# Optimization experiments

Hardware: AMD Instinct MI355X
Metric: run time of the kernel (lower is better)

Reference implementation:

```python
import jax, jax.numpy as jnp
import numpy as np

D_MODEL = 1024
N_HEADS = 16
D_K = D_MODEL // N_HEADS
THETA = 10000.0
B, S = 4, 2048


def setup_inputs() -> dict:
    key = jax.random.key(0)
    ks = jax.random.split(key, 5)
    scale = 0.02
    return {
        "x": jax.random.normal(ks[0], (B, S, D_MODEL), dtype=jnp.float32),
        "token_positions": jnp.arange(S, dtype=jnp.int32),
        "WQ": jax.random.normal(ks[1], (D_MODEL, D_MODEL), dtype=jnp.float32) * scale,
        "WK": jax.random.normal(ks[2], (D_MODEL, D_MODEL), dtype=jnp.float32) * scale,
        "WV": jax.random.normal(ks[3], (D_MODEL, D_MODEL), dtype=jnp.float32) * scale,
        "WO": jax.random.normal(ks[4], (D_MODEL, D_MODEL), dtype=jnp.float32) * scale,
    }


def apply_rope(x, positions):
    # x: [B, H, S, d_k]; rotate interleaved (even, odd) pairs
    half = D_K // 2
    inv_freq = THETA ** (-jnp.arange(half, dtype=x.dtype) * 2.0 / D_K)  # [half]
    ang = positions.astype(x.dtype)[:, None] * inv_freq[None, :]        # [S, half]
    cos, sin = jnp.cos(ang), jnp.sin(ang)
    x1 = x[..., 0::2]
    x2 = x[..., 1::2]
    r1 = x1 * cos - x2 * sin
    r2 = x1 * sin + x2 * cos
    return jnp.stack([r1, r2], axis=-1).reshape(x.shape)


def reference(x, token_positions, WQ, WK, WV, WO):
    b, s, _ = x.shape
    # Linear (no bias), weight stored (out, in): y = x @ W^T
    def proj(W):
        y = jnp.einsum('bsd,ed->bse', x, W)
        return y.reshape(b, s, N_HEADS, D_K).transpose(0, 2, 1, 3)  # [b,h,s,dk]
    Q, K, V = proj(WQ), proj(WK), proj(WV)
    Q = apply_rope(Q, token_positions)
    K = apply_rope(K, token_positions)
    scores = jnp.einsum('bhqd,bhkd->bhqk', Q, K) / jnp.sqrt(jnp.asarray(D_K, x.dtype))
    causal = jnp.tril(jnp.ones((s, s), dtype=bool))
    scores = jnp.where(causal, scores, -jnp.inf)
    attn = jax.nn.softmax(scores, axis=-1)
    out = jnp.einsum('bhqk,bhkd->bhqd', attn, V)
    out = out.transpose(0, 2, 1, 3).reshape(b, s, D_MODEL)
    return jnp.einsum('bse,de->bsd', out, WO)
```

## Files before the change

kernel.cpp:

```cpp
#include <hip/hip_runtime.h>
#include <cstdint>
#include <cstddef>

#define DM 1024
#define NH 16
#define DKD 64
#define BB 4
#define SS 2048
#define MTOT (BB*SS)

typedef float  f32x4  __attribute__((ext_vector_type(4)));
typedef __bf16 bf16x8 __attribute__((ext_vector_type(8)));
typedef __bf16 bf16x4v __attribute__((ext_vector_type(4)));
typedef __bf16 bf16x2v __attribute__((ext_vector_type(2)));
using as3v = __attribute__((address_space(3))) void;
using as1v = __attribute__((address_space(1))) void;

__device__ __forceinline__ void gl2lds16(const void* g, void* l) {
  __builtin_amdgcn_global_load_lds((as1v*)g, (as3v*)l, 16, 0, 0);
}

__device__ __forceinline__ float fast_exp2(float x) {
#if __has_builtin(__builtin_amdgcn_exp2f)
  return __builtin_amdgcn_exp2f(x);
#else
  return __expf(x * 0.6931471805599453f);
#endif
}

__device__ __forceinline__ void sincos_rev(float rev, float* s, float* c) {
#if __has_builtin(__builtin_amdgcn_sinf) && __has_builtin(__builtin_amdgcn_cosf)
  *s = __builtin_amdgcn_sinf(rev);
  *c = __builtin_amdgcn_cosf(rev);
#else
  float a = rev * 6.283185307179586f;
  *s = __sinf(a); *c = __cosf(a);
#endif
}

__device__ __forceinline__ uint32_t pkbf(float a, float b) {
  union { uint32_t u; __bf16 h[2]; } c;
  c.h[0] = (__bf16)a; c.h[1] = (__bf16)b;
  return c.u;
}

__global__ void cast_all_k(const float* __restrict__ x,
                           const float* __restrict__ wq, const float* __restrict__ wk,
                           const float* __restrict__ wv, const float* __restrict__ wo,
                           __bf16* __restrict__ xb,
                           __bf16* __restrict__ wqb, __bf16* __restrict__ wkb,
                           __bf16* __restrict__ wvb, __bf16* __restrict__ wob) {
  int i = blockIdx.x * blockDim.x + threadIdx.x;
  const float* src;
  __bf16* dst;
  int idx, oidx;
  if (i < 2097152) {
    src = x; dst = xb; idx = i; oidx = i;
  } else {
    int j = i - 2097152;
    int w = j >> 18;
    idx = j & 262143;
    src = (w == 0) ? wq : (w == 1) ? wk : (w == 2) ? wv : wo;
    dst = (w == 0) ? wqb : (w == 1) ? wkb : (w == 2) ? wvb : wob;
    if (w < 2) {
      int e = idx >> 8;
      int c = idx & 255;
      int d = e & 63;
      int dp = (d & 1) ? 32 + (d >> 1) : (d >> 1);
      oidx = (((e & ~63) | dp) << 8) | c;
    } else {
      oidx = idx;
    }
  }
  float4 f = ((const float4*)src)[idx];
  bf16x4v o;
  o[0] = (__bf16)f.x; o[1] = (__bf16)f.y; o[2] = (__bf16)f.z; o[3] = (__bf16)f.w;
  ((bf16x4v*)dst)[oidx] = o;
}

__global__ void rope_tbl_k(const int* __restrict__ pos, float2* __restrict__ tbl) {
  int p = blockIdx.x * blockDim.x + threadIdx.x;
  int s = p >> 5;
  int i = p & 31;
  float ps = (float)pos[s];
  float invr = __expf(-0.28782313663f * (float)i) * 0.15915494309f;
  float rev = ps * invr;
  rev -= floorf(rev);
  float sn, cs;
  sincos_rev(rev, &sn, &cs);
  tbl[p] = make_float2(cs, sn);
}

template <typename CT>
__global__ __launch_bounds__(256) void gemm_bt_k(const __bf16* __restrict__ A,
                                                 const __bf16* __restrict__ B,
                                                 CT* __restrict__ C,
                                                 int M, int N, int K) {
  __shared__ __bf16 As[128 * 32];
  __shared__ __bf16 Bs[128 * 32];
  const int tid  = threadIdx.x;
  const int lane = tid & 63;
  const int wid  = tid >> 6;
  const int lrow = lane & 15;
  const int quad = lane >> 4;
  const int m0 = blockIdx.y * 128;
  const int n0 = blockIdx.x * 128;
  const int wm = (wid & 1) * 64;
  const int wn = (wid >> 1) * 64;
  const int srow = wid * 32 + (lane >> 2);
  const int scol = (lane & 3) * 8;

  f32x4 acc[4][4] = {};

  for (int k0 = 0; k0 < K; k0 += 32) {
    __syncthreads();
    gl2lds16(A + (size_t)(m0 + srow)      * K + k0 + scol, As + (wid * 32)      * 32);
    gl2lds16(A + (size_t)(m0 + srow + 16) * K + k0 + scol, As + (wid * 32 + 16) * 32);
    gl2lds16(B + (size_t)(n0 + srow)      * K + k0 + scol, Bs + (wid * 32)      * 32);
    gl2lds16(B + (size_t)(n0 + srow + 16) * K + k0 + scol, Bs + (wid * 32 + 16) * 32);
    __syncthreads();

    bf16x8 af[4], bfr[4];
#pragma unroll
    for (int i = 0; i < 4; ++i)
      af[i] = *(const bf16x8*)(As + (wm + i * 16 + lrow) * 32 + quad * 8);
#pragma unroll
    for (int i = 0; i < 4; ++i)
      bfr[i] = *(const bf16x8*)(Bs + (wn + i * 16 + lrow) * 32 + quad * 8);
#pragma unroll
    for (int mi = 0; mi < 4; ++mi)
#pragma unroll
      for (int ni = 0; ni < 4; ++ni)
        acc[mi][ni] = __builtin_amdgcn_mfma_f32_16x16x32_bf16(af[mi], bfr[ni], acc[mi][ni], 0, 0, 0);
  }

#pragma unroll
  for (int mi = 0; mi < 4; ++mi)
#pragma unroll
    for (int ni = 0; ni < 4; ++ni)
#pragma unroll
      for (int r = 0; r < 4; ++r) {
        int row = m0 + wm + mi * 16 + quad * 4 + r;
        int col = n0 + wn + ni * 16 + lrow;
        C[(size_t)row * N + col] = (CT)acc[mi][ni][r];
      }
}

__global__ __launch_bounds__(256) void gemm_qkv_k(const __bf16* __restrict__ A,
                                                  const __bf16* __restrict__ Bq,
                                                  const __bf16* __restrict__ Bk,
                                                  const __bf16* __restrict__ Bv,
                                                  const float2* __restrict__ tbl,
                                                  __bf16* __restrict__ Cq,
                                                  __bf16* __restrict__ Ck,
                                                  __bf16* __restrict__ Cv) {
  __shared__ __bf16 As[128 * 32];
  __shared__ __bf16 Bs[128 * 32];
  const int sel = blockIdx.x >> 3;
  const __bf16* B = sel == 0 ? Bq : sel == 1 ? Bk : Bv;
  const int n0 = (blockIdx.x & 7) * 128;
  const int m0 = blockIdx.y * 128;
  const int K = DM;
  const int tid  = threadIdx.x;
  const int lane = tid & 63;
  const int wid  = tid >> 6;
  const int lrow = lane & 15;
  const int quad = lane >> 4;
  const int wm = (wid & 1) * 64;
  const int wn = (wid >> 1) * 64;
  const int srow = wid * 32 + (lane >> 2);
  const int scol = (lane & 3) * 8;

  f32x4 acc[4][4] = {};

  for (int k0 = 0; k0 < K; k0 += 32) {
    __syncthreads();
    gl2lds16(A + (size_t)(m0 + srow)      * K + k0 + scol, As + (wid * 32)      * 32);
    gl2lds16(A + (size_t)(m0 + srow + 16) * K + k0 + scol, As + (wid * 32 + 16) * 32);
    gl2lds16(B + (size_t)(n0 + srow)      * K + k0 + scol, Bs + (wid * 32)      * 32);
    gl2lds16(B + (size_t)(n0 + srow + 16) * K + k0 + scol, Bs + (wid * 32 + 16) * 32);
    __syncthreads();

    bf16x8 af[4], bfr[4];
#pragma unroll
    for (int i = 0; i < 4; ++i)
      af[i] = *(const bf16x8*)(As + (wm + i * 16 + lrow) * 32 + quad * 8);
#pragma unroll
    for (int i = 0; i < 4; ++i)
      bfr[i] = *(const bf16x8*)(Bs + (wn + i * 16 + lrow) * 32 + quad * 8);
#pragma unroll
    for (int mi = 0; mi < 4; ++mi)
#pragma unroll
      for (int ni = 0; ni < 4; ++ni)
        acc[mi][ni] = __builtin_amdgcn_mfma_f32_16x16x32_bf16(af[mi], bfr[ni], acc[mi][ni], 0, 0, 0);
  }

  const int hbase = (n0 + wn) >> 6;
  const int bq = m0 >> 11;

  if (sel == 2) {
    __bf16* vt = Cv + ((size_t)(bq * NH + hbase)) * (DKD * SS);
    const int S0 = (m0 + wm) & (SS - 1);
#pragma unroll
    for (int ni = 0; ni < 4; ++ni) {
      const int d = ni * 16 + lrow;
#pragma unroll
      for (int mi = 0; mi < 4; ++mi) {
        bf16x4v pk;
#pragma unroll
        for (int r = 0; r < 4; ++r) pk[r] = (__bf16)acc[mi][ni][r];
        const int sp = S0 + (mi >> 1) * 32 + quad * 8 + (mi & 1) * 4;
        *(bf16x4v*)(vt + (size_t)d * SS + sp) = pk;
      }
    }
  } else {
    __bf16* C = ((sel == 0) ? Cq : Ck) + ((size_t)(bq * NH + hbase)) * (SS * DKD);
#pragma unroll
    for (int ni = 0; ni < 2; ++ni) {
      const int i = ni * 16 + lrow;
#pragma unroll
      for (int mi = 0; mi < 4; ++mi) {
#pragma unroll
        for (int r = 0; r < 4; ++r) {
          int s = (m0 + wm + mi * 16 + quad * 4 + r) & (SS - 1);
          float2 cssn = tbl[s * 32 + i];
          float a = acc[mi][ni][r];
          float b = acc[mi][ni + 2][r];
          C[(size_t)s * DKD + i]      = (__bf16)fmaf(a, cssn.x, -(b * cssn.y));
          C[(size_t)s * DKD + 32 + i] = (__bf16)fmaf(a, cssn.y,  (b * cssn.x));
        }
      }
    }
  }
}

__global__ __launch_bounds__(512, 4) void attn9_k(const __bf16* __restrict__ Qh,
                                                  const __bf16* __restrict__ Kh,
                                                  const __bf16* __restrict__ VT,
                                                  __bf16* __restrict__ O) {
  __shared__ __bf16 Ks[2][128 * 64];
  __shared__ __bf16 Vt[2][64 * 128];
  const int tid  = threadIdx.x;
  const int lane = tid & 63;
  const int wid  = tid >> 6;
  const int lrow = lane & 15;
  const int quad = lane >> 4;
  const int j   = blockIdx.x;
  const int xcd = j & 7;
  const int t   = j >> 3;
  const int bh  = (xcd << 3) | (t >> 4);
  const int u   = t & 15;
  const int qi  = (u & 1) ? (u >> 1) : (15 - (u >> 1));
  const int b  = bh >> 4;
  const int h  = bh & 15;
  const int q0 = qi * 128;
  const size_t hb = (size_t)bh * (SS * DKD);
  const int qg = q0 + wid * 16 + lrow;

  bf16x8 qf0, qf1;
  {
    const __bf16* qp = Qh + hb + (size_t)qg * DKD + quad * 8;
    qf0 = *(const bf16x8*)qp;
    qf1 = *(const bf16x8*)(qp + 32);
  }
  f32x4 Oa[4] = {};
  float l = 0.f;
  const int nkt = qi + 1;

  const int skr = lane >> 3;
  const int skc = lane & 7;
  const int svd = lane >> 4;
  const int svc = lane & 15;

  auto stage = [&](int kt, int bsel) {
#pragma unroll
    for (int ii = 0; ii < 2; ++ii) {
      int i = wid * 2 + ii;
      int key = i * 8 + skr;
      int gc = skc ^ (key & 7);
      gl2lds16(Kh + hb + (size_t)(kt * 128 + key) * DKD + gc * 8, &Ks[bsel][i * 512]);
      int dk = i * 4 + svd;
      int gc2 = (svc & 8) | ((svc ^ dk) & 7);
      gl2lds16(VT + hb + (size_t)dk * SS + kt * 128 + gc2 * 8, &Vt[bsel][i * 512]);
    }
  };

  stage(0, 0);

  for (int kt = 0; kt < nkt; ++kt) {
    __syncthreads();
    if (kt + 1 < nkt) stage(kt + 1, (kt + 1) & 1);
    const __bf16* ks = Ks[kt & 1];
    const __bf16* vt = Vt[kt & 1];

    f32x4 sa[8];
#pragma unroll
    for (int mi = 0; mi < 8; ++mi) sa[mi] = (f32x4){0.f, 0.f, 0.f, 0.f};
    __builtin_amdgcn_s_setprio(1);
#pragma unroll
    for (int tt = 0; tt < 2; ++tt) {
      bf16x8 qf = tt ? qf1 : qf0;
#pragma unroll
      for (int mi = 0; mi < 8; ++mi) {
        bf16x8 kf = *(const bf16x8*)(ks + (mi * 16 + lrow) * 64 + (((tt * 4 + quad) ^ (lrow & 7)) * 8));
        sa[mi] = __builtin_amdgcn_mfma_f32_16x16x32_bf16(kf, qf, sa[mi], 0, 0, 0);
      }
    }
    __builtin_amdgcn_s_setprio(0);

    const bool lastt = (kt == nkt - 1);
#pragma unroll
    for (int kc = 0; kc < 4; ++kc) {
      union { uint32_t u[4]; bf16x8 v; } P;
#pragma unroll
      for (int half = 0; half < 2; ++half) {
        const int mi = kc * 2 + half;
        float pr[4];
#pragma unroll
        for (int r = 0; r < 4; ++r) {
          float p = fast_exp2(sa[mi][r] * 0.18033688f - 8.0f);
          if (lastt) {
            int key = kt * 128 + kc * 32 + half * 16 + quad * 4 + r;
            p = (key <= qg) ? p : 0.f;
          }
          l += p;
          pr[r] = p;
        }
        P.u[half * 2]     = pkbf(pr[0], pr[1]);
        P.u[half * 2 + 1] = pkbf(pr[2], pr[3]);
      }
      __builtin_amdgcn_s_setprio(1);
#pragma unroll
      for (int ni = 0; ni < 4; ++ni) {
        int c = kc * 4 + quad;
        int cp = (c & 8) | ((c ^ (lrow & 7)) & 7);
        bf16x8 vf = *(const bf16x8*)(vt + (ni * 16 + lrow) * 128 + cp * 8);
        Oa[ni] = __builtin_amdgcn_mfma_f32_16x16x32_bf16(P.v, vf, Oa[ni], 0, 0, 0);
      }
      __builtin_amdgcn_s_setprio(0);
    }
  }

  l += __shfl_xor(l, 16, 64);
  l += __shfl_xor(l, 32, 64);

#pragma unroll
  for (int r = 0; r < 4; ++r) {
    float li = __shfl(l, quad * 4 + r, 64);
    float inv = 1.0f / li;
    int row = q0 + wid * 16 + quad * 4 + r;
#pragma unroll
    for (int ni = 0; ni < 4; ++ni)
      O[(size_t)b * SS * DM + (size_t)row * DM + h * DKD + ni * 16 + lrow] =
          (__bf16)(Oa[ni][r] * inv);
  }
}

extern "C" void kernel_launch(void* const* d_in, const int* in_sizes, int n_in,
                              void* d_out, int out_size, void* d_ws, size_t ws_size,
                              hipStream_t stream) {
  (void)in_sizes; (void)n_in; (void)out_size; (void)ws_size;
  const float* x  = (const float*)d_in[0];
  const int*   pos = (const int*)d_in[1];
  const float* WQ = (const float*)d_in[2];
  const float* WK = (const float*)d_in[3];
  const float* WV = (const float*)d_in[4];
  const float* WO = (const float*)d_in[5];
  float* out = (float*)d_out;

  char* w = (char*)d_ws;
  const size_t MB = 1024 * 1024;
  __bf16* xb  = (__bf16*)(w);
  __bf16* wqb = (__bf16*)(w + 16 * MB);
  __bf16* wkb = (__bf16*)(w + 18 * MB);
  __bf16* wvb = (__bf16*)(w + 20 * MB);
  __bf16* wob = (__bf16*)(w + 22 * MB);
  __bf16* Qh  = (__bf16*)(w + 24 * MB);
  __bf16* Kh  = (__bf16*)(w + 40 * MB);
  __bf16* Cb  = (__bf16*)(w + 56 * MB);
  __bf16* VT  = (__bf16*)(w + 72 * MB);
  float2* tbl = (float2*)(w + 88 * MB);

  cast_all_k<<<3145728 / 256, 256, 0, stream>>>(x, WQ, WK, WV, WO, xb, wqb, wkb, wvb, wob);

  rope_tbl_k<<<(SS * 32) / 256, 256, 0, stream>>>(pos, tbl);

  gemm_qkv_k<<<dim3(24, MTOT / 128), 256, 0, stream>>>(xb, wqb, wkb, wvb, tbl, Qh, Kh, VT);

  attn9_k<<<dim3(1024), 512, 0, stream>>>(Qh, Kh, VT, Cb);

  gemm_bt_k<float><<<dim3(DM / 128, MTOT / 128), 256, 0, stream>>>(Cb, wob, out, MTOT, DM, DM);
}
```

Baseline: 282.2 us.

## Pair causal query tiles per block for balanced attention work

Each attention block now handles two query tiles (qi and 15-qi), so every block processes exactly 17 key tiles, and the grid is halved to 512 blocks. The K/V double-buffer prefetch runs continuously across both segments, so the second tile's first load overlaps the first tile's last compute. The row-sum is also split into two partial accumulators. This removes the causal triangle's load imbalance and per-block prologue cost, at the price of fewer blocks (less latency hiding from occupancy) and a longer serial chain per block.

```diff
diff --git a/kernel.cpp b/kernel.cpp
--- a/kernel.cpp
+++ b/kernel.cpp
@@ -234,10 +234,10 @@
   }
 }
 
-__global__ __launch_bounds__(512, 4) void attn9_k(const __bf16* __restrict__ Qh,
-                                                  const __bf16* __restrict__ Kh,
-                                                  const __bf16* __restrict__ VT,
-                                                  __bf16* __restrict__ O) {
+__global__ __launch_bounds__(512, 4) void attn10_k(const __bf16* __restrict__ Qh,
+                                                   const __bf16* __restrict__ Kh,
+                                                   const __bf16* __restrict__ VT,
+                                                   __bf16* __restrict__ O) {
   __shared__ __bf16 Ks[2][128 * 64];
   __shared__ __bf16 Vt[2][64 * 128];
   const int tid  = threadIdx.x;
@@ -248,24 +248,14 @@
   const int j   = blockIdx.x;
   const int xcd = j & 7;
   const int t   = j >> 3;
-  const int bh  = (xcd << 3) | (t >> 4);
-  const int u   = t & 15;
-  const int qi  = (u & 1) ? (u >> 1) : (15 - (u >> 1));
+  const int bh  = (xcd << 3) | (t >> 3);
+  const int pr  = t & 7;
+  const int qa  = pr;
+  const int qb  = 15 - pr;
+  const int na  = qa + 1;
   const int b  = bh >> 4;
   const int h  = bh & 15;
-  const int q0 = qi * 128;
   const size_t hb = (size_t)bh * (SS * DKD);
-  const int qg = q0 + wid * 16 + lrow;
-
-  bf16x8 qf0, qf1;
-  {
-    const __bf16* qp = Qh + hb + (size_t)qg * DKD + quad * 8;
-    qf0 = *(const bf16x8*)qp;
-    qf1 = *(const bf16x8*)(qp + 32);
-  }
-  f32x4 Oa[4] = {};
-  float l = 0.f;
-  const int nkt = qi + 1;
 
   const int skr = lane >> 3;
   const int skc = lane & 7;
@@ -286,73 +276,98 @@
   };
 
   stage(0, 0);
-
-  for (int kt = 0; kt < nkt; ++kt) {
-    __syncthreads();
-    if (kt + 1 < nkt) stage(kt + 1, (kt + 1) & 1);
-    const __bf16* ks = Ks[kt & 1];
-    const __bf16* vt = Vt[kt & 1];
-
-    f32x4 sa[8];
-#pragma unroll
-    for (int mi = 0; mi < 8; ++mi) sa[mi] = (f32x4){0.f, 0.f, 0.f, 0.f};
-    __builtin_amdgcn_s_setprio(1);
-#pragma unroll
-    for (int tt = 0; tt < 2; ++tt) {
-      bf16x8 qf = tt ? qf1 : qf0;
-#pragma unroll
-      for (int mi = 0; mi < 8; ++mi) {
-        bf16x8 kf = *(const bf16x8*)(ks + (mi * 16 + lrow) * 64 + (((tt * 4 + quad) ^ (lrow & 7)) * 8));
-        sa[mi] = __builtin_amdgcn_mfma_f32_16x16x32_bf16(kf, qf, sa[mi], 0, 0, 0);
-      }
-    }
-    __builtin_amdgcn_s_setprio(0);
-
-    const bool lastt = (kt == nkt - 1);
-#pragma unroll
-    for (int kc = 0; kc < 4; ++kc) {
-      union { uint32_t u[4]; bf16x8 v; } P;
-#pragma unroll
-      for (int half = 0; half < 2; ++half) {
-        const int mi = kc * 2 + half;
-        float pr[4];
-#pragma unroll
-        for (int r = 0; r < 4; ++r) {
-          float p = fast_exp2(sa[mi][r] * 0.18033688f - 8.0f);
-          if (lastt) {
-            int key = kt * 128 + kc * 32 + half * 16 + quad * 4 + r;
-            p = (key <= qg) ? p : 0.f;
+  int it = 0;
+
+  for (int seg = 0; seg < 2; ++seg) {
+    const int qi  = seg ? qb : qa;
+    const int q0  = qi * 128;
+    const int nkt = qi + 1;
+    const int qg  = q0 + wid * 16 + lrow;
+
+    bf16x8 qf0, qf1;
+    {
+      const __bf16* qp = Qh + hb + (size_t)qg * DKD + quad * 8;
+      qf0 = *(const bf16x8*)qp;
+      qf1 = *(const bf16x8*)(qp + 32);
+    }
+    f32x4 Oa[4] = {};
+    float la = 0.f, lb = 0.f;
+
+    for (int kt = 0; kt < nkt; ++kt, ++it) {
+      __syncthreads();
+      {
+        int nit = it + 1;
+        if (nit < 17) {
+          int nk = (nit < na) ? nit : (nit - na);
+          stage(nk, nit & 1);
+        }
+      }
+      const __bf16* ks = Ks[it & 1];
+      const __bf16* vt = Vt[it & 1];
+
+      f32x4 sa[8];
+#pragma unroll
+      for (int mi = 0; mi < 8; ++mi) sa[mi] = (f32x4){0.f, 0.f, 0.f, 0.f};
+      __builtin_amdgcn_s_setprio(1);
+#pragma unroll
+      for (int tt = 0; tt < 2; ++tt) {
+        bf16x8 qf = tt ? qf1 : qf0;
+#pragma unroll
+        for (int mi = 0; mi < 8; ++mi) {
+          bf16x8 kf = *(const bf16x8*)(ks + (mi * 16 + lrow) * 64 + (((tt * 4 + quad) ^ (lrow & 7)) * 8));
+          sa[mi] = __builtin_amdgcn_mfma_f32_16x16x32_bf16(kf, qf, sa[mi], 0, 0, 0);
+        }
+      }
+      __builtin_amdgcn_s_setprio(0);
+
+      const bool lastt = (kt == nkt - 1);
+#pragma unroll
+      for (int kc = 0; kc < 4; ++kc) {
+        union { uint32_t u[4]; bf16x8 v; } P;
+#pragma unroll
+        for (int half = 0; half < 2; ++half) {
+          const int mi = kc * 2 + half;
+          float pr4[4];
+#pragma unroll
+          for (int r = 0; r < 4; ++r) {
+            float p = fast_exp2(sa[mi][r] * 0.18033688f - 8.0f);
+            if (lastt) {
+              int key = kt * 128 + kc * 32 + half * 16 + quad * 4 + r;
+              p = (key <= qg) ? p : 0.f;
+            }
+            pr4[r] = p;
           }
-          l += p;
-          pr[r] = p;
+          float s01 = pr4[0] + pr4[1];
+          float s23 = pr4[2] + pr4[3];
+          if (half) lb += (s01 + s23); else la += (s01 + s23);
+          P.u[half * 2]     = pkbf(pr4[0], pr4[1]);
+          P.u[half * 2 + 1] = pkbf(pr4[2], pr4[3]);
         }
-        P.u[half * 2]     = pkbf(pr[0], pr[1]);
-        P.u[half * 2 + 1] = pkbf(pr[2], pr[3]);
-      }
-      __builtin_amdgcn_s_setprio(1);
-#pragma unroll
-      for (int ni = 0; ni < 4; ++ni) {
-        int c = kc * 4 + quad;
-        int cp = (c & 8) | ((c ^ (lrow & 7)) & 7);
-        bf16x8 vf = *(const bf16x8*)(vt + (ni * 16 + lrow) * 128 + cp * 8);
-        Oa[ni] = __builtin_amdgcn_mfma_f32_16x16x32_bf16(P.v, vf, Oa[ni], 0, 0, 0);
-      }
-      __builtin_amdgcn_s_setprio(0);
-    }
-  }
-
-  l += __shfl_xor(l, 16, 64);
-  l += __shfl_xor(l, 32, 64);
-
-#pragma unroll
-  for (int r = 0; r < 4; ++r) {
-    float li = __shfl(l, quad * 4 + r, 64);
-    float inv = 1.0f / li;
-    int row = q0 + wid * 16 + quad * 4 + r;
-#pragma unroll
-    for (int ni = 0; ni < 4; ++ni)
-      O[(size_t)b * SS * DM + (size_t)row * DM + h * DKD + ni * 16 + lrow] =
-          (__bf16)(Oa[ni][r] * inv);
+        __builtin_amdgcn_s_setprio(1);
+#pragma unroll
+        for (int ni = 0; ni < 4; ++ni) {
+          int c = kc * 4 + quad;
+          int cp = (c & 8) | ((c ^ (lrow & 7)) & 7);
+          bf16x8 vf = *(const bf16x8*)(vt + (ni * 16 + lrow) * 128 + cp * 8);
+          Oa[ni] = __builtin_amdgcn_mfma_f32_16x16x32_bf16(P.v, vf, Oa[ni], 0, 0, 0);
+        }
+        __builtin_amdgcn_s_setprio(0);
+      }
+    }
+
+    float l = la + lb;
+    l += __shfl_xor(l, 16, 64);
+    l += __shfl_xor(l, 32, 64);
+#pragma unroll
+    for (int r = 0; r < 4; ++r) {
+      float li = __shfl(l, quad * 4 + r, 64);
+      float inv = 1.0f / li;
+      int row = q0 + wid * 16 + quad * 4 + r;
+#pragma unroll
+      for (int ni = 0; ni < 4; ++ni)
+        O[(size_t)b * SS * DM + (size_t)row * DM + h * DKD + ni * 16 + lrow] =
+            (__bf16)(Oa[ni][r] * inv);
+    }
   }
 }
 
@@ -387,7 +402,7 @@
 
   gemm_qkv_k<<<dim3(24, MTOT / 128), 256, 0, stream>>>(xb, wqb, wkb, wvb, tbl, Qh, Kh, VT);
 
-  attn9_k<<<dim3(1024), 512, 0, stream>>>(Qh, Kh, VT, Cb);
+  attn10_k<<<dim3(512), 512, 0, stream>>>(Qh, Kh, VT, Cb);
 
   gemm_bt_k<float><<<dim3(DM / 128, MTOT / 128), 256, 0, stream>>>(Cb, wob, out, MTOT, DM, DM);
 }
```

Result: faster. 256.1 us (-9.2%).
